# Optimization experiments

Measured on AMD Instinct MI355X. Metric: run time of the kernel, lower is better.

Reference implementation:

```python
import jax, jax.numpy as jnp
import numpy as np

B = 8192; NPG = 32; N = B * NPG; E = 4 * N
F_IN = 70; HEADS = 2; HOUT = 64; D = HEADS * HOUT; NB = 4; REL = 86; DK = D // 2
NEG_SLOPE = 0.2; EPS = 1e-5


def setup_inputs():
    key = jax.random.key(0)
    ks = list(jax.random.split(key, 32)); ki = iter(ks)
    def nk():
        return next(ki)
    def rn(shape, s=0.1):
        return jax.random.normal(nk(), shape, jnp.float32) * s
    base = (jnp.arange(E) // (E // B)) * NPG  # each graph owns a contiguous node range
    def edges():
        s = base + jax.random.randint(nk(), (E,), 0, NPG)
        d = base + jax.random.randint(nk(), (E,), 0, NPG)
        return jnp.stack([s, d]).astype(jnp.int32)
    return dict(
        xh=rn((N, F_IN), 1.0), xt=rn((N, F_IN), 1.0),
        edge_h=edges(), edge_t=edges(),
        batch=(jnp.arange(N) // NPG).astype(jnp.int32),
        rels=jax.random.randint(nk(), (B,), 0, REL).astype(jnp.int32),
        W0=rn((F_IN, D)), Wr=rn((NB - 1, D, D)),
        att_src=rn((NB, HEADS, HOUT)), att_dst=rn((NB, HEADS, HOUT)),
        gat_b=jnp.zeros((NB, D), jnp.float32),
        sag_rel_w=rn((NB, D)), sag_rel_b=jnp.zeros((NB,), jnp.float32),
        sag_root_w=rn((NB, D)),
        nw=jnp.ones((NB, D), jnp.float32), nb2=jnp.zeros((NB, D), jnp.float32),
        inw=jnp.ones((F_IN,), jnp.float32), inb=jnp.zeros((F_IN,), jnp.float32),
        wq=rn((D, DK)), wk=rn((D, DK)),
        cob=jnp.zeros((DK,), jnp.float32), coa=rn((DK,)),
        rel_emb=rn((REL, D * D)),
    )


def _lnorm(x, w, b):  # PyG LayerNorm, node mode (per-node over features)
    mu = jnp.mean(x, -1, keepdims=True)
    var = jnp.var(x, -1, keepdims=True)
    return (x - mu) * jax.lax.rsqrt(var + EPS) * w + b


def _gat(x, src, dst, W, a_s, a_d, bias):
    # src/dst already include self-loops (PyG GATConv default add_self_loops=True)
    h = (x @ W).reshape(N, HEADS, HOUT)
    a_src = jnp.einsum('nhc,hc->nh', h, a_s)
    a_dst = jnp.einsum('nhc,hc->nh', h, a_d)
    alpha = jax.nn.leaky_relu(a_src[src] + a_dst[dst], NEG_SLOPE)  # [E+N, H]
    m = jax.ops.segment_max(alpha, dst, num_segments=N)
    ex = jnp.exp(alpha - m[dst])
    den = jax.ops.segment_sum(ex, dst, num_segments=N)
    w = ex / (den[dst] + 1e-16)
    out = jax.ops.segment_sum(h[src] * w[:, :, None], dst, num_segments=N)
    return out.reshape(N, D) + bias


def _readout(x, ei, batch, rw, rb, root_w):
    # SAGPooling(min_score=-1): GraphConv score, per-graph softmax, keeps all nodes
    aggr = jax.ops.segment_sum(x[ei[0]], ei[1], num_segments=N)
    score = aggr @ rw + rb + x @ root_w  # [N]
    m = jax.ops.segment_max(score, batch, num_segments=B)
    ex = jnp.exp(score - m[batch])
    den = jax.ops.segment_sum(ex, batch, num_segments=B)
    s = ex / (den[batch] + 1e-16)
    return jax.ops.segment_sum(x * s[:, None], batch, num_segments=B)  # global_add_pool [B, D]


def _l2norm(x):
    return x / jnp.clip(jnp.linalg.norm(x, axis=-1, keepdims=True), 1e-12)


def _forward(xh, xt, edge_h, edge_t, batch, rels, W0, Wr, att_src, att_dst, gat_b,
             sag_rel_w, sag_rel_b, sag_root_w, nw, nb2, inw, inb, wq, wk, cob, coa, rel_emb):
    loops = jnp.arange(N, dtype=edge_h.dtype)
    def side(x, ei):
        src = jnp.concatenate([ei[0], loops])
        dst = jnp.concatenate([ei[1], loops])
        x = _lnorm(x, inw, inb)
        reprs = []
        for i in range(NB):
            W = W0 if i == 0 else Wr[i - 1]
            x = _gat(x, src, dst, W, att_src[i], att_dst[i], gat_b[i])
            reprs.append(_readout(x, ei, batch, sag_rel_w[i], sag_rel_b[i], sag_root_w[i]))
            x = jax.nn.elu(_lnorm(x, nw[i], nb2[i]))
        return jnp.stack(reprs, axis=-2)  # [B, NB, D]

    rh = side(xh, edge_h)
    rt = side(xt, edge_t)

    # CoAttentionLayer(receiver=heads, attendant=tails)
    keys = rh @ wk       # [B, NB, DK]
    queries = rt @ wq    # [B, NB, DK]
    att = jnp.tanh(keys[:, :, None, :] + queries[:, None, :, :] + cob) @ coa  # [B, NB, NB]

    # RESCAL
    r = _l2norm(rel_emb[rels]).reshape(B, D, D)
    h = _l2norm(rh)
    t = _l2norm(rt)
    scores = jnp.einsum('bid,bde,bje->bij', h, r, t)
    return jnp.sum(att * scores, axis=(-2, -1))  # [B]


def reference(xh, xt, edge_h, edge_t, batch, rels, W0, Wr, att_src, att_dst, gat_b,
              sag_rel_w, sag_rel_b, sag_root_w, nw, nb2, inw, inb, wq, wk, cob, coa, rel_emb):
    return _forward(xh, xt, edge_h, edge_t, batch, rels, W0, Wr, att_src, att_dst, gat_b,
                    sag_rel_w, sag_rel_b, sag_root_w, nw, nb2, inw, inb, wq, wk, cob, coa, rel_emb)
```

## Files before the change

### kernel.cpp

```cpp
#include <hip/hip_runtime.h>
#include <math.h>

#define NG 8192
#define NPG 32
#define NN (NG*NPG)
#define NE (NN*4)
#define EPG 128
#define NEL (EPG+NPG)
#define FIN 70
#define DIM 128
#define XS 132
#define TS 36
#define NB 4
#define DK 64
#define NREL 86

typedef __attribute__((ext_vector_type(8))) short short8;
typedef __attribute__((ext_vector_type(4))) float f32x4;
typedef __attribute__((ext_vector_type(4))) unsigned int u32x4;

__device__ inline unsigned cvtpk(float a, float b) {
  unsigned r;
  asm("v_cvt_pk_bf16_f32 %0, %1, %2" : "=v"(r) : "v"(a), "v"(b));
  return r;
}
__device__ inline float lo16f(unsigned u) { return __uint_as_float(u << 16); }
__device__ inline float hi16f(unsigned u) { return __uint_as_float(u & 0xffff0000u); }
__device__ inline float bf16f(unsigned short h) {
  return __uint_as_float(((unsigned int)h) << 16);
}

__device__ inline void split8(const f32x4& a, const f32x4& b, short8& hi, short8& lo) {
  u32x4 H, L;
  #pragma unroll
  for (int p = 0; p < 2; ++p) {
    float x0 = a[2*p], x1 = a[2*p+1];
    unsigned h = cvtpk(x0, x1);
    H[p] = h;
    L[p] = cvtpk(x0 - lo16f(h), x1 - hi16f(h));
  }
  #pragma unroll
  for (int p = 0; p < 2; ++p) {
    float x0 = b[2*p], x1 = b[2*p+1];
    unsigned h = cvtpk(x0, x1);
    H[2+p] = h;
    L[2+p] = cvtpk(x0 - lo16f(h), x1 - hi16f(h));
  }
  hi = __builtin_bit_cast(short8, H);
  lo = __builtin_bit_cast(short8, L);
}

__device__ inline short8 ld8(const unsigned short* p) {
  union { short8 s; uint2 u[2]; } U;
  U.u[0] = *(const uint2*)p;
  U.u[1] = *(const uint2*)(p + 4);
  return U.s;
}
__device__ inline short8 ld16B(const unsigned short* p) {
  u32x4 u = *(const u32x4*)p;
  return __builtin_bit_cast(short8, u);
}

struct Smem {
  float x[NPG][XS];
  unsigned short h2thi[DIM][TS];
  unsigned short h2tlo[DIM][TS];
  union {
    float Pt[2][NPG][TS];
    struct {
      float keysl[NB][DK];
      float querl[NB][DK];
      float attw[NB*NB];
      float red[NB*NB];
      float u4[4][DIM];
    } f;
  } uu;
  int   srcl[EPG];
  int   dstl[EPG];
  float asrc[NPG][2];
  float adst[NPG][2];
  float wred[4][2];
  float pl[NPG];
  float ql[NPG];
  float hrq[4][NPG];
  float pqp[2][NPG];
  float pqq[2][NPG];
  float cbl[NB];
  float sval[NPG];
  float sacc[NPG];
  float repr[2][NB][DIM];
  float scl[2][NB];
};

__global__ __launch_bounds__(256) void relnorm_kernel(
    const float* __restrict__ re, float* __restrict__ outn) {
  int r = blockIdx.x;
  const float* row = re + (size_t)r * (DIM*DIM);
  float s = 0.f;
  for (int i = threadIdx.x; i < DIM*DIM; i += 256) { float v = row[i]; s += v*v; }
  for (int w = 1; w < 64; w <<= 1) s += __shfl_xor(s, w);
  __shared__ float sred[4];
  if ((threadIdx.x & 63) == 0) sred[threadIdx.x >> 6] = s;
  __syncthreads();
  if (threadIdx.x == 0) outn[r] = sqrtf(sred[0]+sred[1]+sred[2]+sred[3]);
}

__global__ __launch_bounds__(256) void wprep_kernel(
    const float* __restrict__ W0, const float* __restrict__ Wr,
    unsigned short* __restrict__ wsp) {
  int idx = blockIdx.x * 256 + threadIdx.x;
  int l = idx >> 14;
  int k = (idx >> 7) & 127;
  int c = idx & 127;
  float v;
  if (l == 0) v = (k < FIN) ? W0[(size_t)k*DIM + c] : 0.f;
  else        v = Wr[(size_t)(l-1)*DIM*DIM + (size_t)k*DIM + c];
  unsigned h = cvtpk(v, 0.f);
  unsigned lo = cvtpk(v - lo16f(h), 0.f);
  int o = (l << 14) + c*128 + k;
  wsp[o] = (unsigned short)h;
  wsp[65536 + o] = (unsigned short)lo;
}

__global__ __launch_bounds__(128) void wxprep_kernel(
    const float* __restrict__ W0, const float* __restrict__ Wr,
    const float* __restrict__ att_src, const float* __restrict__ att_dst,
    const float* __restrict__ srw, const float* __restrict__ sroot,
    unsigned short* __restrict__ wx) {
  int b = blockIdx.x;
  int li = b >> 4, j = b & 15;
  int k = threadIdx.x;
  const int K = (li == 0) ? FIN : DIM;
  float val = 0.f;
  if (j < 8 && k < K) {
    const float* Wrow = (li == 0) ? (W0 + (size_t)k*DIM)
                                  : (Wr + (size_t)(li-1)*DIM*DIM + (size_t)k*DIM);
    const float* v; int c0;
    switch (j) {
      case 0: v = att_src + ((size_t)li*2+0)*64; c0 = 0;  break;
      case 1: v = att_dst + ((size_t)li*2+0)*64; c0 = 0;  break;
      case 2: v = att_src + ((size_t)li*2+1)*64; c0 = 64; break;
      case 3: v = att_dst + ((size_t)li*2+1)*64; c0 = 64; break;
      case 4: v = srw   + (size_t)li*DIM;        c0 = 0;  break;
      case 5: v = srw   + (size_t)li*DIM;        c0 = 64; break;
      case 6: v = sroot + (size_t)li*DIM;        c0 = 0;  break;
      default: v = sroot + (size_t)li*DIM;       c0 = 64; break;
    }
    for (int c = 0; c < 64; ++c) {
      float vc = (j < 4) ? v[c] : v[c0 + c];
      val += Wrow[c0 + c] * vc;
    }
  }
  unsigned h = cvtpk(val, 0.f);
  unsigned lo = cvtpk(val - lo16f(h), 0.f);
  int o = (li << 11) + j*128 + k;
  wx[o] = (unsigned short)h;
  wx[8192 + o] = (unsigned short)lo;
}

template <bool FAST>
__global__ __launch_bounds__(256, 3) void ssi_kernel(
    const float* __restrict__ xh, const float* __restrict__ xt,
    const int* __restrict__ eh, const int* __restrict__ et,
    const int* __restrict__ rels,
    const float* __restrict__ W0, const float* __restrict__ Wr,
    const unsigned short* __restrict__ wsp,
    const unsigned short* __restrict__ wx,
    const float* __restrict__ att_src, const float* __restrict__ att_dst,
    const float* __restrict__ gat_b,
    const float* __restrict__ srw, const float* __restrict__ srb,
    const float* __restrict__ sroot,
    const float* __restrict__ nw, const float* __restrict__ nb2,
    const float* __restrict__ inw, const float* __restrict__ inb,
    const float* __restrict__ wqm, const float* __restrict__ wkm,
    const float* __restrict__ cob, const float* __restrict__ coa,
    const float* __restrict__ rel_emb, const float* __restrict__ rnorm,
    float* __restrict__ out)
{
  __shared__ Smem sm;
  const int t = threadIdx.x;
  const int g = blockIdx.x;
  const int n0 = g * NPG;
  const int lw = t & 63;
  const int r0 = lw & 15;
  const int g4 = lw >> 4;
  const int nb = (t >> 6) * 32;
  const int hdw = t >> 7;

  for (int side = 0; side < 2; ++side) {
    const float* xin = side ? xt : xh;
    const int*   ed  = side ? et : eh;

    if (t < EPG) {
      sm.srcl[t] = ed[g*EPG + t] - n0;
      sm.dstl[t] = ed[NE + g*EPG + t] - n0;
    }
    if (FAST && side == 0 && t >= 128) {
      int li2 = (t-128) >> 5, ln = (t-128) & 31;
      float s_ = 0.f;
      #pragma unroll
      for (int m = 0; m < 4; ++m) {
        int c = ln + 32*m;
        s_ += gat_b[(size_t)li2*DIM + c] * srw[(size_t)li2*DIM + c];
      }
      for (int w = 1; w < 32; w <<= 1) s_ += __shfl_xor(s_, w);
      if (ln == 0) sm.cbl[li2] = s_;
    }
    {
      int n = t >> 3, j = t & 7;
      float s = 0.f, s2 = 0.f;
      for (int f = j; f < FIN; f += 8) {
        float v = xin[(size_t)(n0+n)*FIN + f];
        s += v; s2 += v*v;
      }
      for (int w = 1; w < 8; w <<= 1) { s += __shfl_xor(s, w); s2 += __shfl_xor(s2, w); }
      float mu  = s * (1.f/FIN);
      float var = s2 * (1.f/FIN) - mu*mu;
      float inv = rsqrtf(var + 1e-5f);
      for (int f = j; f < FIN; f += 8) {
        float v = xin[(size_t)(n0+n)*FIN + f];
        sm.x[n][f] = (v - mu) * inv * inw[f] + inb[f];
      }
      for (int f = FIN + j; f < 96; f += 8) sm.x[n][f] = 0.f;
    }
    __syncthreads();

    for (int li = 0; li < NB; ++li) {
      {
        const float* W = (li == 0) ? W0 : (Wr + (size_t)(li-1)*DIM*DIM);
        const int K  = (li == 0) ? FIN : DIM;
        const int KS = (li == 0) ? 3 : 4;
        f32x4 acc[2][2];
        f32x4 accx[2];
        #pragma unroll
        for (int mt = 0; mt < 2; ++mt) {
          accx[mt] = (f32x4){0.f,0.f,0.f,0.f};
          #pragma unroll
          for (int nt = 0; nt < 2; ++nt)
            acc[mt][nt] = (f32x4){0.f,0.f,0.f,0.f};
        }
        const unsigned short* Wxh = FAST ? (wx + (li << 11)) : nullptr;
        const unsigned short* Wxl = FAST ? (wx + 8192 + (li << 11)) : nullptr;
        for (int ks = 0; ks < KS; ++ks) {
          const int k0 = ks*32 + g4*8;
          short8 ah[2], al[2], bh[2], bl[2];
          #pragma unroll
          for (int mt = 0; mt < 2; ++mt) {
            f32x4 va = *(const f32x4*)&sm.x[mt*16 + r0][k0];
            f32x4 vb = *(const f32x4*)&sm.x[mt*16 + r0][k0+4];
            split8(va, vb, ah[mt], al[mt]);
          }
          if (wsp) {
            const unsigned short* Wh = wsp + (li << 14);
            const unsigned short* Wl = wsp + 65536 + (li << 14);
            #pragma unroll
            for (int nt = 0; nt < 2; ++nt) {
              const int c = nb + nt*16 + r0;
              bh[nt] = ld16B(Wh + c*128 + k0);
              bl[nt] = ld16B(Wl + c*128 + k0);
            }
          } else {
            #pragma unroll
            for (int nt = 0; nt < 2; ++nt) {
              const int c = nb + nt*16 + r0;
              f32x4 wa, wb;
              #pragma unroll
              for (int j = 0; j < 4; ++j) {
                int ka = k0 + j, kb = k0 + 4 + j;
                wa[j] = (ka < K) ? W[(size_t)ka*DIM + c] : 0.f;
                wb[j] = (kb < K) ? W[(size_t)kb*DIM + c] : 0.f;
              }
              split8(wa, wb, bh[nt], bl[nt]);
            }
          }
          #pragma unroll
          for (int mt = 0; mt < 2; ++mt)
            #pragma unroll
            for (int nt = 0; nt < 2; ++nt) {
              acc[mt][nt] = __builtin_amdgcn_mfma_f32_16x16x32_bf16(ah[mt], bh[nt], acc[mt][nt], 0,0,0);
              acc[mt][nt] = __builtin_amdgcn_mfma_f32_16x16x32_bf16(ah[mt], bl[nt], acc[mt][nt], 0,0,0);
              acc[mt][nt] = __builtin_amdgcn_mfma_f32_16x16x32_bf16(al[mt], bh[nt], acc[mt][nt], 0,0,0);
              acc[mt][nt] = __builtin_amdgcn_mfma_f32_16x16x32_bf16(al[mt], bl[nt], acc[mt][nt], 0,0,0);
            }
          if (FAST && t < 64) {
            short8 bxh = ld16B(Wxh + r0*128 + k0);
            short8 bxl = ld16B(Wxl + r0*128 + k0);
            #pragma unroll
            for (int mt = 0; mt < 2; ++mt) {
              accx[mt] = __builtin_amdgcn_mfma_f32_16x16x32_bf16(ah[mt], bxh, accx[mt], 0,0,0);
              accx[mt] = __builtin_amdgcn_mfma_f32_16x16x32_bf16(ah[mt], bxl, accx[mt], 0,0,0);
              accx[mt] = __builtin_amdgcn_mfma_f32_16x16x32_bf16(al[mt], bxh, accx[mt], 0,0,0);
              accx[mt] = __builtin_amdgcn_mfma_f32_16x16x32_bf16(al[mt], bxl, accx[mt], 0,0,0);
            }
          }
        }
        #pragma unroll
        for (int mt = 0; mt < 2; ++mt)
          #pragma unroll
          for (int nt = 0; nt < 2; ++nt) {
            const int c = nb + nt*16 + r0;
            const int row0 = mt*16 + g4*4;
            f32x4 a = acc[mt][nt];
            unsigned h0 = cvtpk(a[0], a[1]), h1 = cvtpk(a[2], a[3]);
            unsigned l0 = cvtpk(a[0]-lo16f(h0), a[1]-hi16f(h0));
            unsigned l1 = cvtpk(a[2]-lo16f(h1), a[3]-hi16f(h1));
            *(uint2*)&sm.h2thi[c][row0] = make_uint2(h0, h1);
            *(uint2*)&sm.h2tlo[c][row0] = make_uint2(l0, l1);
          }
        if (FAST && t < 64 && r0 < 8) {
          #pragma unroll
          for (int mt = 0; mt < 2; ++mt)
            #pragma unroll
            for (int q = 0; q < 4; ++q) {
              int n = mt*16 + g4*4 + q;
              float v = accx[mt][q];
              switch (r0) {
                case 0: sm.asrc[n][0] = v; break;
                case 1: sm.adst[n][0] = v; break;
                case 2: sm.asrc[n][1] = v; break;
                case 3: sm.adst[n][1] = v; break;
                default: sm.hrq[r0-4][n] = v;
              }
            }
        }
      }
      __syncthreads();

      if (!FAST) {
        int n = t >> 3, hd = (t >> 2) & 1, j = t & 3;
        const float* as = att_src + ((size_t)li*2 + hd)*64;
        const float* ad = att_dst + ((size_t)li*2 + hd)*64;
        float ss = 0.f, sd = 0.f;
        #pragma unroll
        for (int u2 = 0; u2 < 16; ++u2) {
          int cl = u2*4 + j;
          int c = hd*64 + cl;
          float hv = bf16f(sm.h2thi[c][n]) + bf16f(sm.h2tlo[c][n]);
          ss += hv * as[cl];
          sd += hv * ad[cl];
        }
        ss += __shfl_xor(ss,1); ss += __shfl_xor(ss,2);
        sd += __shfl_xor(sd,1); sd += __shfl_xor(sd,2);
        if (j == 0) { sm.asrc[n][hd] = ss; sm.adst[n][hd] = sd; }
        float* Pz = &sm.uu.Pt[0][0][0];
        for (int idx = t; idx < 2*NPG*TS; idx += 256) Pz[idx] = 0.f;
        __syncthreads();
      }

      float al0 = -1e30f, al1 = -1e30f;
      int es = 0, edd = 0;
      if (t < NEL) {
        es  = (t < EPG) ? sm.srcl[t] : (t - EPG);
        edd = (t < EPG) ? sm.dstl[t] : (t - EPG);
        float a0 = sm.asrc[es][0] + sm.adst[edd][0];
        float a1 = sm.asrc[es][1] + sm.adst[edd][1];
        al0 = (a0 > 0.f) ? a0 : 0.2f*a0;
        al1 = (a1 > 0.f) ? a1 : 0.2f*a1;
      }
      if (FAST) {
        float* Pz = &sm.uu.Pt[0][0][0];
        for (int idx = t; idx < 2*NPG*TS; idx += 256) Pz[idx] = 0.f;
      }
      {
        float m0 = al0, m1 = al1;
        for (int w = 1; w < 64; w <<= 1) {
          m0 = fmaxf(m0, __shfl_xor(m0, w));
          m1 = fmaxf(m1, __shfl_xor(m1, w));
        }
        if ((t & 63) == 0) { sm.wred[t>>6][0] = m0; sm.wred[t>>6][1] = m1; }
      }
      __syncthreads();

      if (t < NEL) {
        float M0 = fmaxf(fmaxf(sm.wred[0][0], sm.wred[1][0]),
                         fmaxf(sm.wred[2][0], sm.wred[3][0]));
        float M1 = fmaxf(fmaxf(sm.wred[0][1], sm.wred[1][1]),
                         fmaxf(sm.wred[2][1], sm.wred[3][1]));
        atomicAdd(&sm.uu.Pt[0][edd][es], __expf(al0 - M0));
        atomicAdd(&sm.uu.Pt[1][edd][es], __expf(al1 - M1));
      } else if (FAST && t < NEL + NPG) {
        sm.sacc[t - NEL] = 0.f;
      }
      __syncthreads();

      {
        int hd = t >> 7, r = (t >> 2) & 31, s0 = (t & 3) * 8;
        f32x4 pa = *(const f32x4*)&sm.uu.Pt[hd][r][s0];
        f32x4 pb = *(const f32x4*)&sm.uu.Pt[hd][r][s0+4];
        float rs = pa[0]+pa[1]+pa[2]+pa[3]+pb[0]+pb[1]+pb[2]+pb[3];
        rs += __shfl_xor(rs, 1);
        rs += __shfl_xor(rs, 2);
        float dv = 1.f / (rs + 1e-16f);
        #pragma unroll
        for (int q = 0; q < 4; ++q) { pa[q] *= dv; pb[q] *= dv; }
        if (FAST) {
          f32x4 h0 = *(const f32x4*)&sm.hrq[hd][s0];
          f32x4 h1 = *(const f32x4*)&sm.hrq[hd][s0+4];
          f32x4 q0 = *(const f32x4*)&sm.hrq[2+hd][s0];
          f32x4 q1 = *(const f32x4*)&sm.hrq[2+hd][s0+4];
          float pp = 0.f, qq = 0.f;
          #pragma unroll
          for (int i = 0; i < 4; ++i) {
            pp += pa[i]*h0[i] + pb[i]*h1[i];
            qq += pa[i]*q0[i] + pb[i]*q1[i];
          }
          pp += __shfl_xor(pp, 1); pp += __shfl_xor(pp, 2);
          qq += __shfl_xor(qq, 1); qq += __shfl_xor(qq, 2);
          if ((t & 3) == 0) { sm.pqp[hd][r] = pp; sm.pqq[hd][r] = qq; }
        }
        __syncthreads();
        unsigned short* Pu = (unsigned short*)&sm.uu.Pt[0][0][0];
        const int LO = 2*NPG*TS;
        int base = (hd*NPG + r)*TS + s0;
        unsigned h0 = cvtpk(pa[0], pa[1]), h1 = cvtpk(pa[2], pa[3]);
        unsigned h2_ = cvtpk(pb[0], pb[1]), h3 = cvtpk(pb[2], pb[3]);
        unsigned l0 = cvtpk(pa[0]-lo16f(h0), pa[1]-hi16f(h0));
        unsigned l1 = cvtpk(pa[2]-lo16f(h1), pa[3]-hi16f(h1));
        unsigned l2 = cvtpk(pb[0]-lo16f(h2_), pb[1]-hi16f(h2_));
        unsigned l3 = cvtpk(pb[2]-lo16f(h3), pb[3]-hi16f(h3));
        *(uint2*)(Pu + base)     = make_uint2(h0, h1);
        *(uint2*)(Pu + base + 4) = make_uint2(h2_, h3);
        *(uint2*)(Pu + LO + base)     = make_uint2(l0, l1);
        *(uint2*)(Pu + LO + base + 4) = make_uint2(l2, l3);
      }
      __syncthreads();

      {
        const unsigned short* Pu = (const unsigned short*)&sm.uu.Pt[0][0][0];
        const int LO = 2*NPG*TS;
        const int k0 = g4*8;
        f32x4 acc[2][2];
        #pragma unroll
        for (int mt = 0; mt < 2; ++mt)
          #pragma unroll
          for (int nt = 0; nt < 2; ++nt)
            acc[mt][nt] = (f32x4){0.f,0.f,0.f,0.f};
        short8 Ah[2], Al[2], Bh[2], Bl[2];
        #pragma unroll
        for (int mt = 0; mt < 2; ++mt) {
          int base = (hdw*NPG + mt*16 + r0)*TS + k0;
          Ah[mt] = ld8(Pu + base);
          Al[mt] = ld8(Pu + LO + base);
        }
        #pragma unroll
        for (int nt = 0; nt < 2; ++nt) {
          const int c = nb + nt*16 + r0;
          Bh[nt] = ld8(&sm.h2thi[c][k0]);
          Bl[nt] = ld8(&sm.h2tlo[c][k0]);
        }
        #pragma unroll
        for (int mt = 0; mt < 2; ++mt)
          #pragma unroll
          for (int nt = 0; nt < 2; ++nt) {
            acc[mt][nt] = __builtin_amdgcn_mfma_f32_16x16x32_bf16(Ah[mt], Bh[nt], acc[mt][nt], 0,0,0);
            acc[mt][nt] = __builtin_amdgcn_mfma_f32_16x16x32_bf16(Ah[mt], Bl[nt], acc[mt][nt], 0,0,0);
            acc[mt][nt] = __builtin_amdgcn_mfma_f32_16x16x32_bf16(Al[mt], Bh[nt], acc[mt][nt], 0,0,0);
          }
        #pragma unroll
        for (int nt = 0; nt < 2; ++nt) {
          const int c = nb + nt*16 + r0;
          float bc = gat_b[(size_t)li*DIM + c];
          #pragma unroll
          for (int mt = 0; mt < 2; ++mt)
            #pragma unroll
            for (int q = 0; q < 4; ++q)
              sm.x[mt*16 + g4*4 + q][c] = acc[mt][nt][q] + bc;
        }
      }
      __syncthreads();

      if (!FAST) {
        int n = t >> 3, j = t & 7;
        const float* rw = srw   + (size_t)li*DIM;
        const float* ro = sroot + (size_t)li*DIM;
        float p = 0.f, q = 0.f;
        #pragma unroll
        for (int u2 = 0; u2 < 16; ++u2) {
          int c = u2*8 + j;
          float xv = sm.x[n][c];
          p += xv * rw[c];
          q += xv * ro[c];
        }
        for (int w = 1; w < 8; w <<= 1) { p += __shfl_xor(p,w); q += __shfl_xor(q,w); }
        if (j == 0) { sm.pl[n] = p; sm.ql[n] = q; }
        if (t < NPG) sm.sacc[t] = 0.f;
        __syncthreads();
      }

      if (t < EPG) {
        int s = sm.srcl[t], d = sm.dstl[t];
        float ps;
        if (FAST) ps = sm.pqp[0][s] + sm.pqp[1][s] + sm.cbl[li];
        else      ps = sm.pl[s];
        atomicAdd(&sm.sacc[d], ps);
      }
      __syncthreads();

      if (t < NPG) {
        float qn = FAST ? (sm.pqq[0][t] + sm.pqq[1][t]) : sm.ql[t];
        float s = sm.sacc[t] + srb[li] + qn;
        float m = s;
        for (int w = 1; w < 32; w <<= 1) m = fmaxf(m, __shfl_xor(m, w));
        float ex = __expf(s - m);
        float dn = ex;
        for (int w = 1; w < 32; w <<= 1) dn += __shfl_xor(dn, w);
        sm.sval[t] = ex / (dn + 1e-16f);
      }
      __syncthreads();

      if (t < DIM) {
        float a = 0.f;
        #pragma unroll 8
        for (int n = 0; n < NPG; ++n) a += sm.x[n][t] * sm.sval[n];
        sm.repr[side][li][t] = a;
      }
      __syncthreads();

      if (li < NB-1) {
        int n = t >> 3, j = t & 7;
        float s = 0.f, s2 = 0.f;
        #pragma unroll
        for (int u2 = 0; u2 < 16; ++u2) {
          float v = sm.x[n][u2*8 + j];
          s += v; s2 += v*v;
        }
        for (int w = 1; w < 8; w <<= 1) { s += __shfl_xor(s,w); s2 += __shfl_xor(s2,w); }
        float mu  = s * (1.f/DIM);
        float var = s2 * (1.f/DIM) - mu*mu;
        float inv = rsqrtf(var + 1e-5f);
        const float* wv = nw  + (size_t)li*DIM;
        const float* bv = nb2 + (size_t)li*DIM;
        #pragma unroll
        for (int u2 = 0; u2 < 16; ++u2) {
          int c = u2*8 + j;
          float v = (sm.x[n][c] - mu) * inv * wv[c] + bv[c];
          sm.x[n][c] = (v > 0.f) ? v : (__expf(v) - 1.f);
        }
        __syncthreads();
      }
    }
  }

  {
    int i2 = t >> 6, k = t & 63;
    float ak = 0.f, aq = 0.f;
    for (int d = 0; d < DIM; ++d) {
      ak += sm.repr[0][i2][d] * wkm[(size_t)d*DK + k];
      aq += sm.repr[1][i2][d] * wqm[(size_t)d*DK + k];
    }
    sm.uu.f.keysl[i2][k] = ak;
    sm.uu.f.querl[i2][k] = aq;
  }
  {
    int sd = t >> 7, i = (t >> 5) & 3, j2 = t & 31;
    float s = 0.f;
    #pragma unroll
    for (int u2 = 0; u2 < 4; ++u2) {
      float v = sm.repr[sd][i][j2*4+u2];
      s += v*v;
    }
    for (int w = 1; w < 32; w <<= 1) s += __shfl_xor(s, w);
    if (j2 == 0) sm.scl[sd][i] = 1.f / fmaxf(sqrtf(s), 1e-12f);
  }
  __syncthreads();

  {
    int pair = t >> 4, kk = t & 15;
    int i = pair >> 2, j = pair & 3;
    float a = 0.f;
    #pragma unroll
    for (int u2 = 0; u2 < 4; ++u2) {
      int k = kk*4+u2;
      a += tanhf(sm.uu.f.keysl[i][k] + sm.uu.f.querl[j][k] + cob[k]) * coa[k];
    }
    for (int w = 1; w < 16; w <<= 1) a += __shfl_xor(a, w);
    if (kk == 0) sm.uu.f.attw[pair] = a;
  }
  int rel = rels[g];
  if (t < DIM) {
    const float* rr = rel_emb + (size_t)rel * (DIM*DIM);
    float a0=0.f, a1=0.f, a2=0.f, a3=0.f;
    for (int d = 0; d < DIM; ++d) {
      float rv = rr[(size_t)d*DIM + t];
      a0 += sm.repr[0][0][d] * rv;
      a1 += sm.repr[0][1][d] * rv;
      a2 += sm.repr[0][2][d] * rv;
      a3 += sm.repr[0][3][d] * rv;
    }
    sm.uu.f.u4[0][t]=a0; sm.uu.f.u4[1][t]=a1; sm.uu.f.u4[2][t]=a2; sm.uu.f.u4[3][t]=a3;
  }
  __syncthreads();

  {
    float rninv = 1.f / fmaxf(rnorm[rel], 1e-12f);
    int pair = t >> 4, kk = t & 15;
    int i = pair >> 2, j = pair & 3;
    float a = 0.f;
    #pragma unroll
    for (int u2 = 0; u2 < 8; ++u2) {
      int e = kk*8+u2;
      a += sm.uu.f.u4[i][e] * sm.repr[1][j][e];
    }
    for (int w = 1; w < 16; w <<= 1) a += __shfl_xor(a, w);
    if (kk == 0)
      sm.uu.f.red[pair] = sm.uu.f.attw[pair] * a * sm.scl[0][i] * sm.scl[1][j] * rninv;
  }
  __syncthreads();
  if (t == 0) {
    float s = 0.f;
    for (int p = 0; p < NB*NB; ++p) s += sm.uu.f.red[p];
    out[g] = s;
  }
}

extern "C" void kernel_launch(void* const* d_in, const int* in_sizes, int n_in,
                              void* d_out, int out_size, void* d_ws, size_t ws_size,
                              hipStream_t stream) {
  const float* xh      = (const float*)d_in[0];
  const float* xt      = (const float*)d_in[1];
  const int*   eh      = (const int*)d_in[2];
  const int*   et      = (const int*)d_in[3];
  const int*   rels    = (const int*)d_in[5];
  const float* W0      = (const float*)d_in[6];
  const float* Wr      = (const float*)d_in[7];
  const float* att_src = (const float*)d_in[8];
  const float* att_dst = (const float*)d_in[9];
  const float* gat_b   = (const float*)d_in[10];
  const float* srw     = (const float*)d_in[11];
  const float* srb     = (const float*)d_in[12];
  const float* sroot   = (const float*)d_in[13];
  const float* nw      = (const float*)d_in[14];
  const float* nb2_    = (const float*)d_in[15];
  const float* inw     = (const float*)d_in[16];
  const float* inb     = (const float*)d_in[17];
  const float* wqm     = (const float*)d_in[18];
  const float* wkm     = (const float*)d_in[19];
  const float* cob     = (const float*)d_in[20];
  const float* coa     = (const float*)d_in[21];
  const float* rel_emb = (const float*)d_in[22];
  float* out   = (float*)d_out;
  float* rnorm = (float*)d_ws;

  const size_t NEED_W    = 512 + (size_t)2*65536*sizeof(unsigned short);
  const size_t NEED_FULL = NEED_W + (size_t)2*8192*sizeof(unsigned short);

  relnorm_kernel<<<NREL, 256, 0, stream>>>(rel_emb, rnorm);

  if (ws_size >= NEED_FULL) {
    unsigned short* wsp = (unsigned short*)((char*)d_ws + 512);
    unsigned short* wx  = wsp + 2*65536;
    wprep_kernel<<<256, 256, 0, stream>>>(W0, Wr, wsp);
    wxprep_kernel<<<64, 128, 0, stream>>>(W0, Wr, att_src, att_dst, srw, sroot, wx);
    ssi_kernel<true><<<NG, 256, 0, stream>>>(xh, xt, eh, et, rels, W0, Wr, wsp, wx,
        att_src, att_dst, gat_b, srw, srb, sroot, nw, nb2_, inw, inb,
        wqm, wkm, cob, coa, rel_emb, rnorm, out);
  } else if (ws_size >= NEED_W) {
    unsigned short* wsp = (unsigned short*)((char*)d_ws + 512);
    wprep_kernel<<<256, 256, 0, stream>>>(W0, Wr, wsp);
    ssi_kernel<false><<<NG, 256, 0, stream>>>(xh, xt, eh, et, rels, W0, Wr, wsp, nullptr,
        att_src, att_dst, gat_b, srw, srb, sroot, nw, nb2_, inw, inb,
        wqm, wkm, cob, coa, rel_emb, rnorm, out);
  } else {
    ssi_kernel<false><<<NG, 256, 0, stream>>>(xh, xt, eh, et, rels, W0, Wr, nullptr, nullptr,
        att_src, att_dst, gat_b, srw, srb, sroot, nw, nb2_, inw, inb,
        wqm, wkm, cob, coa, rel_emb, rnorm, out);
  }
}
```

Baseline: 1.230 ms.

## Fuse SAG readout into GAT MFMA epilogue and cut block barriers

```diff
diff --git a/kernel.cpp b/kernel.cpp
--- a/kernel.cpp
+++ b/kernel.cpp
@@ -378,7 +378,7 @@
                          fmaxf(sm.wred[2][1], sm.wred[3][1]));
         atomicAdd(&sm.uu.Pt[0][edd][es], __expf(al0 - M0));
         atomicAdd(&sm.uu.Pt[1][edd][es], __expf(al1 - M1));
-      } else if (FAST && t < NEL + NPG) {
+      } else if (t < NEL + NPG) {
         sm.sacc[t - NEL] = 0.f;
       }
       __syncthreads();
@@ -422,19 +422,23 @@
         *(uint2*)(Pu + base + 4) = make_uint2(h2_, h3);
         *(uint2*)(Pu + LO + base)     = make_uint2(l0, l1);
         *(uint2*)(Pu + LO + base + 4) = make_uint2(l2, l3);
+        if (FAST && t < EPG) {
+          int s = sm.srcl[t], d = sm.dstl[t];
+          atomicAdd(&sm.sacc[d], sm.pqp[0][s] + sm.pqp[1][s] + sm.cbl[li]);
+        }
       }
       __syncthreads();
 
+      f32x4 acc5[2][2];
       {
         const unsigned short* Pu = (const unsigned short*)&sm.uu.Pt[0][0][0];
         const int LO = 2*NPG*TS;
         const int k0 = g4*8;
-        f32x4 acc[2][2];
         #pragma unroll
         for (int mt = 0; mt < 2; ++mt)
           #pragma unroll
           for (int nt = 0; nt < 2; ++nt)
-            acc[mt][nt] = (f32x4){0.f,0.f,0.f,0.f};
+            acc5[mt][nt] = (f32x4){0.f,0.f,0.f,0.f};
         short8 Ah[2], Al[2], Bh[2], Bl[2];
         #pragma unroll
         for (int mt = 0; mt < 2; ++mt) {
@@ -452,69 +456,96 @@
         for (int mt = 0; mt < 2; ++mt)
           #pragma unroll
           for (int nt = 0; nt < 2; ++nt) {
-            acc[mt][nt] = __builtin_amdgcn_mfma_f32_16x16x32_bf16(Ah[mt], Bh[nt], acc[mt][nt], 0,0,0);
-            acc[mt][nt] = __builtin_amdgcn_mfma_f32_16x16x32_bf16(Ah[mt], Bl[nt], acc[mt][nt], 0,0,0);
-            acc[mt][nt] = __builtin_amdgcn_mfma_f32_16x16x32_bf16(Al[mt], Bh[nt], acc[mt][nt], 0,0,0);
-          }
+            acc5[mt][nt] = __builtin_amdgcn_mfma_f32_16x16x32_bf16(Ah[mt], Bh[nt], acc5[mt][nt], 0,0,0);
+            acc5[mt][nt] = __builtin_amdgcn_mfma_f32_16x16x32_bf16(Ah[mt], Bl[nt], acc5[mt][nt], 0,0,0);
+            acc5[mt][nt] = __builtin_amdgcn_mfma_f32_16x16x32_bf16(Al[mt], Bh[nt], acc5[mt][nt], 0,0,0);
+          }
+        if (!FAST) {
+          #pragma unroll
+          for (int nt = 0; nt < 2; ++nt) {
+            const int c = nb + nt*16 + r0;
+            float bc = gat_b[(size_t)li*DIM + c];
+            #pragma unroll
+            for (int mt = 0; mt < 2; ++mt)
+              #pragma unroll
+              for (int q = 0; q < 4; ++q)
+                sm.x[mt*16 + g4*4 + q][c] = acc5[mt][nt][q] + bc;
+          }
+        }
+        if (FAST && t < NPG) {
+          float s = sm.sacc[t] + srb[li] + sm.pqq[0][t] + sm.pqq[1][t];
+          float m = s;
+          for (int w = 1; w < 32; w <<= 1) m = fmaxf(m, __shfl_xor(m, w));
+          float ex = __expf(s - m);
+          float dn = ex;
+          for (int w = 1; w < 32; w <<= 1) dn += __shfl_xor(dn, w);
+          sm.sval[t] = ex / (dn + 1e-16f);
+        }
+      }
+      __syncthreads();
+
+      if (FAST) {
+        float sv[2][4];
+        #pragma unroll
+        for (int mt = 0; mt < 2; ++mt)
+          #pragma unroll
+          for (int q = 0; q < 4; ++q)
+            sv[mt][q] = sm.sval[mt*16 + g4*4 + q];
         #pragma unroll
         for (int nt = 0; nt < 2; ++nt) {
           const int c = nb + nt*16 + r0;
           float bc = gat_b[(size_t)li*DIM + c];
+          float pr = 0.f;
           #pragma unroll
           for (int mt = 0; mt < 2; ++mt)
             #pragma unroll
-            for (int q = 0; q < 4; ++q)
-              sm.x[mt*16 + g4*4 + q][c] = acc[mt][nt][q] + bc;
-        }
-      }
-      __syncthreads();
-
-      if (!FAST) {
-        int n = t >> 3, j = t & 7;
-        const float* rw = srw   + (size_t)li*DIM;
-        const float* ro = sroot + (size_t)li*DIM;
-        float p = 0.f, q = 0.f;
-        #pragma unroll
-        for (int u2 = 0; u2 < 16; ++u2) {
-          int c = u2*8 + j;
-          float xv = sm.x[n][c];
-          p += xv * rw[c];
-          q += xv * ro[c];
-        }
-        for (int w = 1; w < 8; w <<= 1) { p += __shfl_xor(p,w); q += __shfl_xor(q,w); }
-        if (j == 0) { sm.pl[n] = p; sm.ql[n] = q; }
-        if (t < NPG) sm.sacc[t] = 0.f;
-        __syncthreads();
-      }
-
-      if (t < EPG) {
-        int s = sm.srcl[t], d = sm.dstl[t];
-        float ps;
-        if (FAST) ps = sm.pqp[0][s] + sm.pqp[1][s] + sm.cbl[li];
-        else      ps = sm.pl[s];
-        atomicAdd(&sm.sacc[d], ps);
-      }
-      __syncthreads();
-
-      if (t < NPG) {
-        float qn = FAST ? (sm.pqq[0][t] + sm.pqq[1][t]) : sm.ql[t];
-        float s = sm.sacc[t] + srb[li] + qn;
-        float m = s;
-        for (int w = 1; w < 32; w <<= 1) m = fmaxf(m, __shfl_xor(m, w));
-        float ex = __expf(s - m);
-        float dn = ex;
-        for (int w = 1; w < 32; w <<= 1) dn += __shfl_xor(dn, w);
-        sm.sval[t] = ex / (dn + 1e-16f);
-      }
-      __syncthreads();
-
-      if (t < DIM) {
-        float a = 0.f;
-        #pragma unroll 8
-        for (int n = 0; n < NPG; ++n) a += sm.x[n][t] * sm.sval[n];
-        sm.repr[side][li][t] = a;
-      }
-      __syncthreads();
+            for (int q = 0; q < 4; ++q) {
+              float xv = acc5[mt][nt][q] + bc;
+              sm.x[mt*16 + g4*4 + q][c] = xv;
+              pr += xv * sv[mt][q];
+            }
+          pr += __shfl_xor(pr, 16);
+          pr += __shfl_xor(pr, 32);
+          if (g4 == 0) sm.repr[side][li][c] = pr;
+        }
+        __syncthreads();
+      } else {
+        {
+          int n = t >> 3, j = t & 7;
+          const float* rw = srw   + (size_t)li*DIM;
+          const float* ro = sroot + (size_t)li*DIM;
+          float p = 0.f, q = 0.f;
+          #pragma unroll
+          for (int u2 = 0; u2 < 16; ++u2) {
+            int c = u2*8 + j;
+            float xv = sm.x[n][c];
+            p += xv * rw[c];
+            q += xv * ro[c];
+          }
+          for (int w = 1; w < 8; w <<= 1) { p += __shfl_xor(p,w); q += __shfl_xor(q,w); }
+          if (j == 0) { sm.pl[n] = p; sm.ql[n] = q; }
+        }
+        __syncthreads();
+        if (t < EPG) atomicAdd(&sm.sacc[sm.dstl[t]], sm.pl[sm.srcl[t]]);
+        __syncthreads();
+        if (t < NPG) {
+          float s = sm.sacc[t] + srb[li] + sm.ql[t];
+          float m = s;
+          for (int w = 1; w < 32; w <<= 1) m = fmaxf(m, __shfl_xor(m, w));
+          float ex = __expf(s - m);
+          float dn = ex;
+          for (int w = 1; w < 32; w <<= 1) dn += __shfl_xor(dn, w);
+          sm.sval[t] = ex / (dn + 1e-16f);
+        }
+        __syncthreads();
+        if (t < DIM) {
+          float a = 0.f;
+          #pragma unroll 8
+          for (int n = 0; n < NPG; ++n) a += sm.x[n][t] * sm.sval[n];
+          sm.repr[side][li][t] = a;
+        }
+        __syncthreads();
+      }
 
       if (li < NB-1) {
         int n = t >> 3, j = t & 7;
```

Measured after the change: 1.212 ms. About the same (-1.5%).
